# Optimization experiments

Hardware: AMD Instinct MI355X
Metric: run time of the kernel (lower is better)

## Reference

```python
import jax, jax.numpy as jnp
import numpy as np

# SpargeAttn / spas_sage2_attn_meansim block sizes
BLKQ, BLKK = 128, 64
NUM_HEADS = 8
SIMTHRESHD1 = 0.6
CDFTHRESHD = 0.98


def _block_meta(t, blk):
    # t: [B,H,S,D] -> block means [B,H,nb,D] and min-cosine-to-mean per block [B,H,nb]
    B, H, S, D = t.shape
    nb = S // blk
    tb = t.reshape(B, H, nb, blk, D)
    m = tb.mean(axis=3)
    tn = tb / (jnp.linalg.norm(tb, axis=-1, keepdims=True) + 1e-6)
    mn = m / (jnp.linalg.norm(m, axis=-1, keepdims=True) + 1e-6)
    cos = jnp.einsum('bhnkd,bhnd->bhnk', tn, mn)
    return m, cos.min(axis=-1)


def _meansim_sparse_attention(q, k, v, scale):
    # Block-sparse attention with mean-similarity pruning (SpargeAttn meansim).
    qm, qsim = _block_meta(q, BLKQ)          # [B,H,nq,D], [B,H,nq]
    km, ksim = _block_meta(k, BLKK)          # [B,H,nk,D], [B,H,nk]
    q_self = qsim > SIMTHRESHD1              # self-similar Q blocks -> mean is representative
    k_self = ksim > SIMTHRESHD1
    # pooled attention map over block means
    pooled = jax.nn.softmax(jnp.einsum('bhqd,bhkd->bhqk', qm, km) * scale, axis=-1)
    # per Q-block row: keep highest-prob K blocks until cumulative mass >= cdfthreshd
    order = jnp.argsort(-pooled, axis=-1)
    sp = jnp.take_along_axis(pooled, order, axis=-1)
    csum = jnp.cumsum(sp, axis=-1)
    keep_sorted = (csum - sp) < CDFTHRESHD   # always keeps at least the top block
    inv = jnp.argsort(order, axis=-1)
    keep = jnp.take_along_axis(keep_sorted, inv, axis=-1)  # [B,H,nq,nk]
    # conservative fallback: non-self-similar Q/K blocks are never pruned
    block_mask = keep | (~q_self)[..., None] | (~k_self)[:, :, None, :]
    tok_mask = jnp.repeat(jnp.repeat(block_mask, BLKQ, axis=2), BLKK, axis=3)
    s = jnp.einsum('bhqd,bhkd->bhqk', q, k) * scale
    s = jnp.where(tok_mask, s, -jnp.inf)
    p = jax.nn.softmax(s, axis=-1)
    return jnp.einsum('bhqk,bhkd->bhqd', p, v)


def setup_inputs() -> dict:
    key = jax.random.key(0)
    B, L, C = 2, 2048, 512
    ks = jax.random.split(key, 3)
    x = jax.random.normal(ks[0], (B, L, C), jnp.float32)
    Wqkv = jax.random.normal(ks[1], (C, 3 * C), jnp.float32) * (C ** -0.5)
    bqkv = jnp.zeros((3 * C,), jnp.float32)
    Wproj = jax.random.normal(ks[2], (C, C), jnp.float32) * (C ** -0.5)
    bproj = jnp.zeros((C,), jnp.float32)
    return {"x": x, "Wqkv": Wqkv, "bqkv": bqkv, "Wproj": Wproj, "bproj": bproj}


def reference(x, Wqkv, bqkv, Wproj, bproj):
    B, L, C = x.shape
    H = NUM_HEADS
    D = C // H
    scale = D ** -0.5
    qkv = (x @ Wqkv + bqkv).reshape(B, L, 3, H, D)
    qkv = jnp.transpose(qkv, (2, 0, 3, 1, 4))  # [3,B,H,L,D]
    q, k, v = qkv[0], qkv[1], qkv[2]
    o = _meansim_sparse_attention(q, k, v, scale)  # [B,H,L,D]
    o = jnp.transpose(o, (0, 2, 1, 3)).reshape(B, L, C)
    return o @ Wproj + bproj
```

## Files before the change

### kernel.cpp

```cpp
#include <hip/hip_runtime.h>
#include <math.h>

typedef unsigned short ushortT;
typedef unsigned int uintT;
typedef __attribute__((ext_vector_type(8))) short short8;
typedef __attribute__((ext_vector_type(16))) float f32x16;
#define MFMA32(a, b, c) __builtin_amdgcn_mfma_f32_32x32x16_bf16((a), (b), (c), 0, 0, 0)


#define LOG2E 1.4426950408889634f

static __device__ __forceinline__ ushortT f2b(float f) {
    union { float f; uintT u; } v; v.f = f;
    uintT u = v.u;
    u += 0x7fffu + ((u >> 16) & 1u);
    return (ushortT)(u >> 16);
}
static __device__ __forceinline__ uintT pack2(float a, float b) {
    return (uintT)f2b(a) | ((uintT)f2b(b) << 16);
}
static __device__ __forceinline__ uintT pack2t(float a, float b) {
    union { float f; uintT u; } x0, x1; x0.f = a; x1.f = b;
    return __builtin_amdgcn_perm(x1.u, x0.u, 0x07060302u);
}
static __device__ __forceinline__ float blo(uintT u) {
    union { uintT u; float f; } v; v.u = u << 16; return v.f;
}
static __device__ __forceinline__ float bhi(uintT u) {
    union { uintT u; float f; } v; v.u = u & 0xffff0000u; return v.f;
}
static __device__ __forceinline__ f32x16 zero16() {
    f32x16 z;
    #pragma unroll
    for (int i = 0; i < 16; ++i) z[i] = 0.f;
    return z;
}

#define B_N 2
#define H_N 8
#define L_N 2048
#define NQB 16
#define NKB 32

__global__ __launch_bounds__(256) void prep_kernel(
    const float* __restrict__ x, ushortT* __restrict__ xb,
    const float* __restrict__ Wq, ushortT* __restrict__ Wqt,
    const float* __restrict__ Wp, ushortT* __restrict__ Wpt) {
    const int bid = blockIdx.x, t = threadIdx.x;
    __shared__ float tile[32][33];
    if (bid < 2048) {
        int i = (bid * 256 + t) * 4;
        float4 v = *(const float4*)(x + i);
        uint2 o; o.x = pack2(v.x, v.y); o.y = pack2(v.z, v.w);
        *(uint2*)(xb + i) = o;
        return;
    }
    const float* W; ushortT* Wt; int C, c0, r0;
    if (bid < 2816) {
        const int b = bid - 2048;
        W = Wq; Wt = Wqt; C = 1536;
        c0 = (b % 48) * 32; r0 = (b / 48) * 32;
    } else {
        const int b = bid - 2816;
        W = Wp; Wt = Wpt; C = 512;
        c0 = (b & 15) * 32; r0 = (b >> 4) * 32;
    }
    const int tx = t & 31, ty = t >> 5;
    #pragma unroll
    for (int i = 0; i < 4; ++i)
        tile[ty + 8 * i][tx] = W[(size_t)(r0 + ty + 8 * i) * C + c0 + tx];
    __syncthreads();
    #pragma unroll
    for (int i = 0; i < 4; ++i) {
        int rr = ty + 8 * i;
        Wt[(size_t)(c0 + rr) * 512 + r0 + tx] = f2b(tile[tx][rr]);
    }
}

__global__ __launch_bounds__(256) void qkv_gemm_kernel(
    const ushortT* __restrict__ xb, const ushortT* __restrict__ wt,
    const float* __restrict__ bias,
    ushortT* __restrict__ qb, ushortT* __restrict__ kbuf, ushortT* __restrict__ vt,
    float* __restrict__ qm, float* __restrict__ km) {
    __shared__ __align__(16) ushortT As[2][128 * 40];
    __shared__ __align__(16) ushortT Bs[2][128 * 40];
    __shared__ float sumbuf[2][128];
    const int t = threadIdx.x;
    const int l = t & 63, w = t >> 6;
    const int lm = l & 31, lh = l >> 5;
    const int wm = w >> 1, wn = w & 1;
    const int rowbase = blockIdx.y * 128;
    const int colbase = blockIdx.x * 128;

    f32x16 acc[2][2];
    acc[0][0] = zero16(); acc[0][1] = zero16();
    acc[1][0] = zero16(); acc[1][1] = zero16();

    const int r = t >> 1, half = t & 1;
    const ushortT* Ag = xb + (size_t)(rowbase + r) * 512 + half * 16;
    const ushortT* Bg = wt + (size_t)(colbase + r) * 512 + half * 16;
    const int so = r * 40 + half * 16;

    uint4 a0, a1, b0, b1;
    a0 = *(const uint4*)(Ag); a1 = *(const uint4*)(Ag + 8);
    b0 = *(const uint4*)(Bg); b1 = *(const uint4*)(Bg + 8);
    *(uint4*)(&As[0][so]) = a0; *(uint4*)(&As[0][so] + 8) = a1;
    *(uint4*)(&Bs[0][so]) = b0; *(uint4*)(&Bs[0][so] + 8) = b1;

    for (int k0 = 0; k0 < 512; k0 += 32) {
        const int cur = (k0 >> 5) & 1;
        __syncthreads();
        if (k0 < 480) {
            a0 = *(const uint4*)(Ag + k0 + 32); a1 = *(const uint4*)(Ag + k0 + 40);
            b0 = *(const uint4*)(Bg + k0 + 32); b1 = *(const uint4*)(Bg + k0 + 40);
        }
        #pragma unroll
        for (int ks = 0; ks < 2; ++ks) {
            const int ko = 16 * ks + 8 * lh;
            short8 a_0 = *(const short8*)(&As[cur][(64 * wm + lm) * 40 + ko]);
            short8 a_1 = *(const short8*)(&As[cur][(64 * wm + 32 + lm) * 40 + ko]);
            short8 b_0 = *(const short8*)(&Bs[cur][(64 * wn + lm) * 40 + ko]);
            short8 b_1 = *(const short8*)(&Bs[cur][(64 * wn + 32 + lm) * 40 + ko]);
            acc[0][0] = MFMA32(a_0, b_0, acc[0][0]);
            acc[0][1] = MFMA32(a_0, b_1, acc[0][1]);
            acc[1][0] = MFMA32(a_1, b_0, acc[1][0]);
            acc[1][1] = MFMA32(a_1, b_1, acc[1][1]);
        }
        if (k0 < 480) {
            const int nxt = cur ^ 1;
            *(uint4*)(&As[nxt][so]) = a0; *(uint4*)(&As[nxt][so] + 8) = a1;
            *(uint4*)(&Bs[nxt][so]) = b0; *(uint4*)(&Bs[nxt][so] + 8) = b1;
        }
    }

    const int which = blockIdx.x >> 2;
    const int by = blockIdx.y;
    const int b = by >> 4;
    float bias2[2];
    int cc[2], hh[2], dd[2];
    #pragma unroll
    for (int nt = 0; nt < 2; ++nt) {
        cc[nt] = colbase + 64 * wn + 32 * nt + lm;
        bias2[nt] = bias[cc[nt]];
        hh[nt] = (cc[nt] >> 6) & 7;
        dd[nt] = cc[nt] & 63;
    }
    float msum[2] = {0.f, 0.f};
    #pragma unroll
    for (int mt = 0; mt < 2; ++mt) {
        #pragma unroll
        for (int nt = 0; nt < 2; ++nt) {
            const size_t hb = (size_t)(b * 8 + hh[nt]);
            #pragma unroll
            for (int rg = 0; rg < 16; ++rg) {
                const int row_local = 64 * wm + 32 * mt + (rg & 3) + 8 * (rg >> 2) + 4 * lh;
                const int token = rowbase + row_local;
                const int ll = token & 2047;
                float val = acc[mt][nt][rg] + bias2[nt];
                if (which == 0) {
                    val *= 0.125f;
                    msum[nt] += val;
                    qb[(hb * 2048 + ll) * 64 + dd[nt]] = f2b(val * LOG2E);
                } else if (which == 1) {
                    msum[nt] += val;
                    kbuf[(hb * 2048 + ll) * 64 + dd[nt]] = f2b(val);
                } else {
                    vt[hb * 131072 + (size_t)(ll >> 6) * 4096 + dd[nt] * 64 + (ll & 63)] = f2b(val);
                }
            }
        }
    }
    if (which == 0) {
        #pragma unroll
        for (int nt = 0; nt < 2; ++nt) {
            float s = msum[nt] + __shfl_xor(msum[nt], 32);
            if (l < 32) sumbuf[wm][64 * wn + 32 * nt + lm] = s;
        }
        __syncthreads();
        if (t < 128) {
            const int c = colbase + t;
            const int h = (c >> 6) & 7, d = c & 63;
            const int qbi = by & 15;
            qm[((size_t)(b * 8 + h) * 16 + qbi) * 64 + d] =
                (sumbuf[0][t] + sumbuf[1][t]) * (1.0f / 128.0f);
        }
    } else if (which == 1) {
        const int kbi = ((by & 15) << 1) | wm;
        #pragma unroll
        for (int nt = 0; nt < 2; ++nt) {
            float s = msum[nt] + __shfl_xor(msum[nt], 32);
            if (l < 32)
                km[((size_t)(b * 8 + hh[nt]) * 32 + kbi) * 64 + dd[nt]] = s * (1.0f / 64.0f);
        }
    }
}

__global__ __launch_bounds__(256) void cos_kernel(const ushortT* __restrict__ qb,
                                                  const ushortT* __restrict__ kbuf,
                                                  const float* __restrict__ qm,
                                                  const float* __restrict__ km,
                                                  float* __restrict__ qs,
                                                  float* __restrict__ ks) {
    const int bh = blockIdx.y, t = threadIdx.x;
    const int l = t & 63, w = t >> 6;
    __shared__ float mS[64];
    __shared__ float wmin[4];
    if (blockIdx.z == 0) {
        if (blockIdx.x >= 16) return;
        const int qbk = blockIdx.x;
        if (t < 64) mS[t] = qm[((size_t)bh * 16 + qbk) * 64 + t];
        __syncthreads();
        float qn = 0.f;
        #pragma unroll
        for (int d = 0; d < 64; ++d) qn += mS[d] * mS[d];
        qn = sqrtf(qn);
        const int tok = t >> 1, half = t & 1;
        const ushortT* qrow = qb + ((size_t)bh * 2048 + qbk * 128 + tok) * 64 + half * 32;
        float dot = 0.f, nn = 0.f;
        #pragma unroll
        for (int c = 0; c < 4; ++c) {
            uint4 u = *(const uint4*)(qrow + c * 8);
            const int db = half * 32 + c * 8;
            float f0 = blo(u.x), f1 = bhi(u.x), f2 = blo(u.y), f3 = bhi(u.y);
            float f4 = blo(u.z), f5 = bhi(u.z), f6 = blo(u.w), f7 = bhi(u.w);
            dot += f0 * mS[db] + f1 * mS[db + 1] + f2 * mS[db + 2] + f3 * mS[db + 3]
                 + f4 * mS[db + 4] + f5 * mS[db + 5] + f6 * mS[db + 6] + f7 * mS[db + 7];
            nn += f0 * f0 + f1 * f1 + f2 * f2 + f3 * f3 + f4 * f4 + f5 * f5 + f6 * f6 + f7 * f7;
        }
        dot += __shfl_xor(dot, 1);
        nn += __shfl_xor(nn, 1);
        float cosv = dot / ((sqrtf(nn) + 1e-6f) * (qn + 1e-6f));
        #pragma unroll
        for (int off = 1; off < 64; off <<= 1) cosv = fminf(cosv, __shfl_xor(cosv, off));
        if (l == 0) wmin[w] = cosv;
        __syncthreads();
        if (t == 0)
            qs[bh * 16 + qbk] = fminf(fminf(wmin[0], wmin[1]), fminf(wmin[2], wmin[3]));
    } else {
        const int kbk = blockIdx.x;
        if (t < 64) mS[t] = km[((size_t)bh * 32 + kbk) * 64 + t];
        __syncthreads();
        float kn = 0.f;
        #pragma unroll
        for (int d = 0; d < 64; ++d) kn += mS[d] * mS[d];
        kn = sqrtf(kn);
        const int tok = t >> 2, quarter = t & 3;
        const ushortT* krow = kbuf + ((size_t)bh * 2048 + kbk * 64 + tok) * 64 + quarter * 16;
        float dot = 0.f, nn = 0.f;
        #pragma unroll
        for (int c = 0; c < 2; ++c) {
            uint4 u = *(const uint4*)(krow + c * 8);
            const int db = quarter * 16 + c * 8;
            float f0 = blo(u.x), f1 = bhi(u.x), f2 = blo(u.y), f3 = bhi(u.y);
            float f4 = blo(u.z), f5 = bhi(u.z), f6 = blo(u.w), f7 = bhi(u.w);
            dot += f0 * mS[db] + f1 * mS[db + 1] + f2 * mS[db + 2] + f3 * mS[db + 3]
                 + f4 * mS[db + 4] + f5 * mS[db + 5] + f6 * mS[db + 6] + f7 * mS[db + 7];
            nn += f0 * f0 + f1 * f1 + f2 * f2 + f3 * f3 + f4 * f4 + f5 * f5 + f6 * f6 + f7 * f7;
        }
        dot += __shfl_xor(dot, 1); dot += __shfl_xor(dot, 2);
        nn += __shfl_xor(nn, 1); nn += __shfl_xor(nn, 2);
        float cosv = dot / ((sqrtf(nn) + 1e-6f) * (kn + 1e-6f));
        #pragma unroll
        for (int off = 1; off < 64; off <<= 1) cosv = fminf(cosv, __shfl_xor(cosv, off));
        if (l == 0) wmin[w] = cosv;
        __syncthreads();
        if (t == 0)
            ks[bh * 32 + kbk] = fminf(fminf(wmin[0], wmin[1]), fminf(wmin[2], wmin[3]));
    }
}

__global__ __launch_bounds__(512) void mask_kernel(const float* __restrict__ qm,
                                                   const float* __restrict__ km,
                                                   const float* __restrict__ qs,
                                                   const float* __restrict__ ks,
                                                   int* __restrict__ maskp) {
    const int bh = blockIdx.x, t = threadIdx.x;
    __shared__ float qmS[16 * 64];
    __shared__ float kmS[32 * 64];
    __shared__ float pooled[16 * 32];
    __shared__ float pnorm[16 * 32];
    for (int i = t; i < 1024; i += 512) qmS[i] = qm[(size_t)bh * 1024 + i];
    for (int i = t; i < 2048; i += 512) kmS[i] = km[(size_t)bh * 2048 + i];
    __syncthreads();
    {
        const int qbi = t >> 5, kbi = t & 31;
        float dot = 0.f;
        #pragma unroll
        for (int d = 0; d < 64; ++d) dot += qmS[qbi * 64 + d] * kmS[kbi * 64 + d];
        pooled[t] = dot;
    }
    __syncthreads();
    if (t < 16) {
        float mx = -1e30f;
        #pragma unroll
        for (int kb = 0; kb < NKB; ++kb) mx = fmaxf(mx, pooled[t * 32 + kb]);
        float sum = 0.f;
        #pragma unroll
        for (int kb = 0; kb < NKB; ++kb) {
            const float e = expf(pooled[t * 32 + kb] - mx);
            pnorm[t * 32 + kb] = e;
            sum += e;
        }
        const float inv = 1.0f / sum;
        #pragma unroll
        for (int kb = 0; kb < NKB; ++kb) pnorm[t * 32 + kb] *= inv;
    }
    __syncthreads();
    {
        const int row = t >> 5, kb = t & 31;
        const float pk = pnorm[row * 32 + kb];
        float before = 0.f;
        #pragma unroll
        for (int j = 0; j < NKB; ++j) {
            const float pj = pnorm[row * 32 + j];
            if (pj > pk || (pj == pk && j < kb)) before += pj;
        }
        const bool keep = before < 0.98f;
        const bool qfb = !(qs[bh * 16 + row] > 0.6f);
        const bool kfb = !(ks[bh * 32 + kb] > 0.6f);
        maskp[((size_t)bh * 16 + row) * 32 + kb] = (keep || qfb || kfb) ? 1 : 0;
    }
}

__global__ __launch_bounds__(256) void attn_kernel(
    const ushortT* __restrict__ qb, const ushortT* __restrict__ kbuf,
    const ushortT* __restrict__ vt, const int* __restrict__ maskp,
    uintT* __restrict__ pc0, uintT* __restrict__ pc1,
    uintT* __restrict__ pc2, uintT* __restrict__ pc3, float* __restrict__ lp) {
    __shared__ __align__(16) ushortT Ks[2][64 * 72];
    __shared__ __align__(16) ushortT Vs[2][64 * 72];
    __shared__ int klist[33];
    const int t = threadIdx.x;
    const int l = t & 63, w = t >> 6;
    const int lm = l & 31, lh = l >> 5;
    const int qt = blockIdx.x, bh = blockIdx.y, kc = blockIdx.z;
    const int NC = gridDim.z;

    if (w == 0) {
        const int* mrow = maskp + ((size_t)bh * 16 + qt) * 32;
        const int keep = (l < 32) ? mrow[l] : 0;
        unsigned long long bal = __ballot(keep != 0);
        if (keep) {
            const int rank = __popcll(bal & ((1ULL << l) - 1ULL));
            klist[rank] = l;
        }
        if (l == 0) klist[32] = __popcll(bal);
    }
    const ushortT* qg = qb + ((size_t)bh * 2048 + qt * 128) * 64;
    short8 qf[4];
    #pragma unroll
    for (int ksd = 0; ksd < 4; ++ksd)
        qf[ksd] = *(const short8*)(qg + (32 * w + lm) * 64 + 16 * ksd + 8 * lh);
    __syncthreads();

    const int cnt = klist[32];
    const int per = cnt / NC, rem = cnt - per * NC;
    const int n = per + (kc < rem ? 1 : 0);
    const int s = kc * per + (kc < rem ? kc : rem);

    const ushortT* kgb = kbuf + (size_t)bh * 2048 * 64;
    const ushortT* vgb = vt + (size_t)bh * 131072;
    const int cr = t >> 3, cp = (t & 7) * 8;
    const int gK0 = cr * 64 + cp, gK1 = gK0 + 2048;
    const int sK0 = cr * 72 + cp, sK1 = sK0 + 2304;

    f32x16 oacc[2];
    oacc[0] = zero16(); oacc[1] = zero16();
    float l_i = 0.f;

    uint4 ka0, ka1, va0, va1;
    if (n > 0) {
        const int kb0 = klist[s];
        const ushortT* kg = kgb + (size_t)kb0 * 4096;
        const ushortT* vg = vgb + (size_t)kb0 * 4096;
        ka0 = *(const uint4*)(kg + gK0); ka1 = *(const uint4*)(kg + gK1);
        va0 = *(const uint4*)(vg + gK0); va1 = *(const uint4*)(vg + gK1);
        *(uint4*)(&Ks[0][sK0]) = ka0; *(uint4*)(&Ks[0][sK1]) = ka1;
        *(uint4*)(&Vs[0][sK0]) = va0; *(uint4*)(&Vs[0][sK1]) = va1;
    }

    for (int i = 0; i < n; ++i) {
        const int cur = i & 1;
        __syncthreads();
        if (i + 1 < n) {
            const int kbn = klist[s + i + 1];
            const ushortT* kg = kgb + (size_t)kbn * 4096;
            const ushortT* vg = vgb + (size_t)kbn * 4096;
            ka0 = *(const uint4*)(kg + gK0); ka1 = *(const uint4*)(kg + gK1);
            va0 = *(const uint4*)(vg + gK0); va1 = *(const uint4*)(vg + gK1);
        }
        f32x16 sacc[2];
        sacc[0] = zero16(); sacc[1] = zero16();
        #pragma unroll
        for (int ksd = 0; ksd < 4; ++ksd) {
            const int ko = 16 * ksd + 8 * lh;
            short8 kf0 = *(const short8*)(&Ks[cur][lm * 72 + ko]);
            short8 kf1 = *(const short8*)(&Ks[cur][(32 + lm) * 72 + ko]);
            sacc[0] = MFMA32(kf0, qf[ksd], sacc[0]);
            sacc[1] = MFMA32(kf1, qf[ksd], sacc[1]);
        }
        float psum0 = 0.f, psum1 = 0.f;
        uintT uu[2][4][2];
        #pragma unroll
        for (int mt = 0; mt < 2; ++mt) {
            #pragma unroll
            for (int rp = 0; rp < 8; ++rp) {
                const float e0 = exp2f(sacc[mt][2 * rp]);
                const float e1 = exp2f(sacc[mt][2 * rp + 1]);
                psum0 += e0; psum1 += e1;
                uu[mt][rp >> 1][rp & 1] = pack2t(e0, e1);
            }
        }
        float psum = psum0 + psum1;
        psum += __shfl_xor(psum, 32);
        l_i += psum;
        #pragma unroll
        for (int ksk = 0; ksk < 4; ++ksk) {
            const int mt = ksk >> 1, par = ksk & 1;
            const uintT kA = lh ? uu[mt][2 * par + 1][0] : uu[mt][2 * par][0];
            const uintT kB = lh ? uu[mt][2 * par + 1][1] : uu[mt][2 * par][1];
            const uintT sA = lh ? uu[mt][2 * par][0] : uu[mt][2 * par + 1][0];
            const uintT sB = lh ? uu[mt][2 * par][1] : uu[mt][2 * par + 1][1];
            const uintT rA = (uintT)__shfl_xor((int)sA, 32);
            const uintT rB = (uintT)__shfl_xor((int)sB, 32);
            union { uintT u[4]; short8 v; } cv;
            if (lh == 0) { cv.u[0] = kA; cv.u[1] = kB; cv.u[2] = rA; cv.u[3] = rB; }
            else         { cv.u[0] = rA; cv.u[1] = rB; cv.u[2] = kA; cv.u[3] = kB; }
            const int ko = 16 * ksk + 8 * lh;
            short8 vf0 = *(const short8*)(&Vs[cur][lm * 72 + ko]);
            short8 vf1 = *(const short8*)(&Vs[cur][(32 + lm) * 72 + ko]);
            oacc[0] = MFMA32(vf0, cv.v, oacc[0]);
            oacc[1] = MFMA32(vf1, cv.v, oacc[1]);
        }
        if (i + 1 < n) {
            const int nxt = cur ^ 1;
            *(uint4*)(&Ks[nxt][sK0]) = ka0; *(uint4*)(&Ks[nxt][sK1]) = ka1;
            *(uint4*)(&Vs[nxt][sK0]) = va0; *(uint4*)(&Vs[nxt][sK1]) = va1;
        }
    }
    if (lh == 0)
        lp[kc * 32768 + ((size_t)bh * 16 + qt) * 128 + 32 * w + lm] = l_i;
    uintT pu[16];
    #pragma unroll
    for (int mt = 0; mt < 2; ++mt)
        #pragma unroll
        for (int rp = 0; rp < 8; ++rp)
            pu[mt * 8 + rp] = pack2(oacc[mt][2 * rp], oacc[mt][2 * rp + 1]);
    uintT* pcb = (kc == 0) ? pc0 : (kc == 1) ? pc1 : (kc == 2) ? pc2 : pc3;
    uintT* pdst = pcb + (((size_t)bh * 16 + qt) * 4 + w) * 1024 + l * 4;
    #pragma unroll
    for (int i4 = 0; i4 < 4; ++i4)
        *(uint4*)(pdst + i4 * 256) =
            make_uint4(pu[i4 * 4], pu[i4 * 4 + 1], pu[i4 * 4 + 2], pu[i4 * 4 + 3]);
}

__global__ __launch_bounds__(256) void reduce_kernel(
    const uintT* __restrict__ pc0, const uintT* __restrict__ pc1,
    const uintT* __restrict__ pc2, const uintT* __restrict__ pc3,
    const float* __restrict__ lp, ushortT* __restrict__ ob, int NC) {
    const int t = threadIdx.x;
    const int l = t & 63, w = t >> 6;
    const int lm = l & 31, lh = l >> 5;
    const int qt = blockIdx.x, bh = blockIdx.y;
    const size_t base = (((size_t)bh * 16 + qt) * 4 + w) * 1024 + l * 4;
    const int qrow = 32 * w + lm;
    float accL[16], accH[16];
    #pragma unroll
    for (int i = 0; i < 16; ++i) { accL[i] = 0.f; accH[i] = 0.f; }
    float lsum = 0.f;
    #pragma unroll
    for (int c = 0; c < 4; ++c) {
        if (c >= NC) break;
        const uintT* p = (c == 0) ? pc0 : (c == 1) ? pc1 : (c == 2) ? pc2 : pc3;
        #pragma unroll
        for (int i4 = 0; i4 < 4; ++i4) {
            uint4 v = *(const uint4*)(p + base + i4 * 256);
            accL[i4 * 4 + 0] += blo(v.x); accH[i4 * 4 + 0] += bhi(v.x);
            accL[i4 * 4 + 1] += blo(v.y); accH[i4 * 4 + 1] += bhi(v.y);
            accL[i4 * 4 + 2] += blo(v.z); accH[i4 * 4 + 2] += bhi(v.z);
            accL[i4 * 4 + 3] += blo(v.w); accH[i4 * 4 + 3] += bhi(v.w);
        }
        lsum += lp[c * 32768 + ((size_t)bh * 16 + qt) * 128 + qrow];
    }
    const float invl = 1.0f / lsum;
    __syncthreads();
    ushortT* orow = ob + ((size_t)bh * 2048 + qt * 128 + qrow) * 64;
    #pragma unroll
    for (int idx = 0; idx < 16; ++idx) {
        const int mt = idx >> 3, rp = idx & 7;
        const int d0 = 32 * mt + 8 * (rp >> 1) + 4 * lh + 2 * (rp & 1);
        *(uintT*)(orow + d0) = pack2(accL[idx] * invl, accH[idx] * invl);
    }
}

__global__ __launch_bounds__(256) void proj_gemm_kernel(
    const ushortT* __restrict__ ob, const ushortT* __restrict__ wpt,
    const float* __restrict__ bias, float* __restrict__ out) {
    __shared__ __align__(16) ushortT As[2][128 * 40];
    __shared__ __align__(16) ushortT Bs[2][64 * 40];
    const int t = threadIdx.x;
    const int l = t & 63, w = t >> 6;
    const int lm = l & 31, lh = l >> 5;
    const int rowbase = blockIdx.y * 128;
    const int colbase = blockIdx.x * 64;

    f32x16 acc[2];
    acc[0] = zero16(); acc[1] = zero16();

    const int r = t >> 1, half = t & 1;
    const int token = rowbase + r;
    const int b2 = token >> 11, lt = token & 2047;
    const int soA = r * 40 + half * 16;
    const ushortT* obbase = ob + ((size_t)(b2 * 8) * 2048 + lt) * 64 + half * 16;
    const int rb = t >> 2, q4 = t & 3;
    const int soB = rb * 40 + q4 * 8;
    const ushortT* Bg = wpt + (size_t)(colbase + rb) * 512 + q4 * 8;

    uint4 a0, a1, b0;
    a0 = *(const uint4*)(obbase); a1 = *(const uint4*)(obbase + 8);
    b0 = *(const uint4*)(Bg);
    *(uint4*)(&As[0][soA]) = a0; *(uint4*)(&As[0][soA] + 8) = a1;
    *(uint4*)(&Bs[0][soB]) = b0;

    for (int k0 = 0; k0 < 512; k0 += 32) {
        const int cur = (k0 >> 5) & 1;
        __syncthreads();
        if (k0 < 480) {
            const int kn = k0 + 32;
            const ushortT* Ag = obbase + (size_t)(kn >> 6) * 131072 + (kn & 63);
            a0 = *(const uint4*)(Ag); a1 = *(const uint4*)(Ag + 8);
            b0 = *(const uint4*)(Bg + kn);
        }
        #pragma unroll
        for (int ks = 0; ks < 2; ++ks) {
            const int ko = 16 * ks + 8 * lh;
            short8 af = *(const short8*)(&As[cur][(32 * w + lm) * 40 + ko]);
            short8 b_0 = *(const short8*)(&Bs[cur][lm * 40 + ko]);
            short8 b_1 = *(const short8*)(&Bs[cur][(32 + lm) * 40 + ko]);
            acc[0] = MFMA32(af, b_0, acc[0]);
            acc[1] = MFMA32(af, b_1, acc[1]);
        }
        if (k0 < 480) {
            const int nxt = cur ^ 1;
            *(uint4*)(&As[nxt][soA]) = a0; *(uint4*)(&As[nxt][soA] + 8) = a1;
            *(uint4*)(&Bs[nxt][soB]) = b0;
        }
    }
    float bias2[2];
    #pragma unroll
    for (int nt = 0; nt < 2; ++nt) bias2[nt] = bias[colbase + 32 * nt + lm];
    #pragma unroll
    for (int nt = 0; nt < 2; ++nt) {
        const int c = colbase + 32 * nt + lm;
        #pragma unroll
        for (int rg = 0; rg < 16; ++rg) {
            const int row_local = 32 * w + (rg & 3) + 8 * (rg >> 2) + 4 * lh;
            out[(size_t)(rowbase + row_local) * 512 + c] = acc[nt][rg] + bias2[nt];
        }
    }
}

extern "C" void kernel_launch(void* const* d_in, const int* in_sizes, int n_in,
                              void* d_out, int out_size, void* d_ws, size_t ws_size,
                              hipStream_t stream) {
    const float* x     = (const float*)d_in[0];
    const float* Wqkv  = (const float*)d_in[1];
    const float* bqkv  = (const float*)d_in[2];
    const float* Wproj = (const float*)d_in[3];
    const float* bproj = (const float*)d_in[4];
    float* out = (float*)d_out;

    char* w = (char*)d_ws;
    ushortT* xb     = (ushortT*)(w);
    ushortT* wqkvt  = (ushortT*)(w + 4194304);
    ushortT* wprojt = (ushortT*)(w + 5767168);
    ushortT* qb     = (ushortT*)(w + 6291456);
    ushortT* kbuf   = (ushortT*)(w + 10485760);
    ushortT* vt     = (ushortT*)(w + 14680064);
    ushortT* ob     = (ushortT*)(w + 18874368);
    float*   qm     = (float*)(w + 23068672);
    float*   km     = (float*)(w + 23134208);
    float*   qs     = (float*)(w + 23265280);
    float*   ks     = (float*)(w + 23266304);
    int*     maskp  = (int*)(w + 23268352);
    float*   lp2    = (float*)(w + 23301120);
    uintT*   pc2    = (uintT*)(w + 23563264);
    uintT*   pc3    = (uintT*)(w + 27757568);
    float*   lp4    = (float*)(w + 31951872);
    const int NC = (ws_size >= 32476160) ? 4 : 2;
    float* lpA = (NC == 4) ? lp4 : lp2;

    uintT* pc0 = (uintT*)xb;
    uintT* pc1 = (uintT*)ob;
    if (NC == 2) { pc2 = pc0; pc3 = pc0; }

    prep_kernel<<<3072, 256, 0, stream>>>(x, xb, Wqkv, wqkvt, Wproj, wprojt);
    qkv_gemm_kernel<<<dim3(12, 32), 256, 0, stream>>>(xb, wqkvt, bqkv, qb, kbuf, vt, qm, km);
    cos_kernel<<<dim3(32, 16, 2), 256, 0, stream>>>(qb, kbuf, qm, km, qs, ks);
    mask_kernel<<<16, 512, 0, stream>>>(qm, km, qs, ks, maskp);
    attn_kernel<<<dim3(16, 16, NC), 256, 0, stream>>>(qb, kbuf, vt, maskp, pc0, pc1, pc2, pc3, lpA);
    reduce_kernel<<<dim3(16, 16), 256, 0, stream>>>(pc0, pc1, pc2, pc3, lpA, ob, NC);
    proj_gemm_kernel<<<dim3(8, 32), 256, 0, stream>>>(ob, wprojt, bproj, out);
}
```

Before: 158.2 us.

## Shrink GEMM tiles, drop LDS staging in attention, swap attention grid order

The QKV GEMM moves from 128x128 to 128x64 tiles, so the grid doubles and each block covers exactly one head, which simplifies the mean-reduction epilogue. The projection GEMM moves to 64x64 tiles with one MFMA accumulator per wave, doubling its grid. The attention kernel drops the double-buffered shared-memory K/V staging and reads K/V fragments directly from global memory, and swaps grid x/y so consecutive blocks share a query tile across heads. The aim is more parallelism and less LDS and sync overhead, at the cost of less data reuse and uncoalesced, unpipelined global loads in attention.

```diff
diff --git a/kernel.cpp b/kernel.cpp
--- a/kernel.cpp
+++ b/kernel.cpp
@@ -83,114 +83,101 @@
     ushortT* __restrict__ qb, ushortT* __restrict__ kbuf, ushortT* __restrict__ vt,
     float* __restrict__ qm, float* __restrict__ km) {
     __shared__ __align__(16) ushortT As[2][128 * 40];
-    __shared__ __align__(16) ushortT Bs[2][128 * 40];
-    __shared__ float sumbuf[2][128];
+    __shared__ __align__(16) ushortT Bs[2][64 * 40];
+    __shared__ float sumbuf[4][64];
     const int t = threadIdx.x;
     const int l = t & 63, w = t >> 6;
     const int lm = l & 31, lh = l >> 5;
-    const int wm = w >> 1, wn = w & 1;
     const int rowbase = blockIdx.y * 128;
-    const int colbase = blockIdx.x * 128;
-
-    f32x16 acc[2][2];
-    acc[0][0] = zero16(); acc[0][1] = zero16();
-    acc[1][0] = zero16(); acc[1][1] = zero16();
+    const int colbase = blockIdx.x * 64;
+
+    f32x16 acc[2];
+    acc[0] = zero16(); acc[1] = zero16();
 
     const int r = t >> 1, half = t & 1;
     const ushortT* Ag = xb + (size_t)(rowbase + r) * 512 + half * 16;
-    const ushortT* Bg = wt + (size_t)(colbase + r) * 512 + half * 16;
-    const int so = r * 40 + half * 16;
-
-    uint4 a0, a1, b0, b1;
+    const int soA = r * 40 + half * 16;
+    const int rb = t >> 2, q4 = t & 3;
+    const ushortT* Bg = wt + (size_t)(colbase + rb) * 512 + q4 * 8;
+    const int soB = rb * 40 + q4 * 8;
+
+    uint4 a0, a1, b0;
     a0 = *(const uint4*)(Ag); a1 = *(const uint4*)(Ag + 8);
-    b0 = *(const uint4*)(Bg); b1 = *(const uint4*)(Bg + 8);
-    *(uint4*)(&As[0][so]) = a0; *(uint4*)(&As[0][so] + 8) = a1;
-    *(uint4*)(&Bs[0][so]) = b0; *(uint4*)(&Bs[0][so] + 8) = b1;
+    b0 = *(const uint4*)(Bg);
+    *(uint4*)(&As[0][soA]) = a0; *(uint4*)(&As[0][soA] + 8) = a1;
+    *(uint4*)(&Bs[0][soB]) = b0;
 
     for (int k0 = 0; k0 < 512; k0 += 32) {
         const int cur = (k0 >> 5) & 1;
         __syncthreads();
         if (k0 < 480) {
             a0 = *(const uint4*)(Ag + k0 + 32); a1 = *(const uint4*)(Ag + k0 + 40);
-            b0 = *(const uint4*)(Bg + k0 + 32); b1 = *(const uint4*)(Bg + k0 + 40);
+            b0 = *(const uint4*)(Bg + k0 + 32);
         }
         #pragma unroll
         for (int ks = 0; ks < 2; ++ks) {
             const int ko = 16 * ks + 8 * lh;
-            short8 a_0 = *(const short8*)(&As[cur][(64 * wm + lm) * 40 + ko]);
-            short8 a_1 = *(const short8*)(&As[cur][(64 * wm + 32 + lm) * 40 + ko]);
-            short8 b_0 = *(const short8*)(&Bs[cur][(64 * wn + lm) * 40 + ko]);
-            short8 b_1 = *(const short8*)(&Bs[cur][(64 * wn + 32 + lm) * 40 + ko]);
-            acc[0][0] = MFMA32(a_0, b_0, acc[0][0]);
-            acc[0][1] = MFMA32(a_0, b_1, acc[0][1]);
-            acc[1][0] = MFMA32(a_1, b_0, acc[1][0]);
-            acc[1][1] = MFMA32(a_1, b_1, acc[1][1]);
+            short8 af  = *(const short8*)(&As[cur][(32 * w + lm) * 40 + ko]);
+            short8 b_0 = *(const short8*)(&Bs[cur][lm * 40 + ko]);
+            short8 b_1 = *(const short8*)(&Bs[cur][(32 + lm) * 40 + ko]);
+            acc[0] = MFMA32(af, b_0, acc[0]);
+            acc[1] = MFMA32(af, b_1, acc[1]);
         }
         if (k0 < 480) {
             const int nxt = cur ^ 1;
-            *(uint4*)(&As[nxt][so]) = a0; *(uint4*)(&As[nxt][so] + 8) = a1;
-            *(uint4*)(&Bs[nxt][so]) = b0; *(uint4*)(&Bs[nxt][so] + 8) = b1;
-        }
-    }
-
-    const int which = blockIdx.x >> 2;
+            *(uint4*)(&As[nxt][soA]) = a0; *(uint4*)(&As[nxt][soA] + 8) = a1;
+            *(uint4*)(&Bs[nxt][soB]) = b0;
+        }
+    }
+
+    const int which = blockIdx.x >> 3;
+    const int h = blockIdx.x & 7;
     const int by = blockIdx.y;
     const int b = by >> 4;
+    const size_t hb = (size_t)(b * 8 + h);
     float bias2[2];
-    int cc[2], hh[2], dd[2];
+    #pragma unroll
+    for (int nt = 0; nt < 2; ++nt) bias2[nt] = bias[colbase + 32 * nt + lm];
+    float msum[2] = {0.f, 0.f};
     #pragma unroll
     for (int nt = 0; nt < 2; ++nt) {
-        cc[nt] = colbase + 64 * wn + 32 * nt + lm;
-        bias2[nt] = bias[cc[nt]];
-        hh[nt] = (cc[nt] >> 6) & 7;
-        dd[nt] = cc[nt] & 63;
-    }
-    float msum[2] = {0.f, 0.f};
-    #pragma unroll
-    for (int mt = 0; mt < 2; ++mt) {
-        #pragma unroll
-        for (int nt = 0; nt < 2; ++nt) {
-            const size_t hb = (size_t)(b * 8 + hh[nt]);
-            #pragma unroll
-            for (int rg = 0; rg < 16; ++rg) {
-                const int row_local = 64 * wm + 32 * mt + (rg & 3) + 8 * (rg >> 2) + 4 * lh;
-                const int token = rowbase + row_local;
-                const int ll = token & 2047;
-                float val = acc[mt][nt][rg] + bias2[nt];
-                if (which == 0) {
-                    val *= 0.125f;
-                    msum[nt] += val;
-                    qb[(hb * 2048 + ll) * 64 + dd[nt]] = f2b(val * LOG2E);
-                } else if (which == 1) {
-                    msum[nt] += val;
-                    kbuf[(hb * 2048 + ll) * 64 + dd[nt]] = f2b(val);
-                } else {
-                    vt[hb * 131072 + (size_t)(ll >> 6) * 4096 + dd[nt] * 64 + (ll & 63)] = f2b(val);
-                }
+        const int dd = 32 * nt + lm;
+        #pragma unroll
+        for (int rg = 0; rg < 16; ++rg) {
+            const int row_local = 32 * w + (rg & 3) + 8 * (rg >> 2) + 4 * lh;
+            const int ll = (rowbase + row_local) & 2047;
+            float val = acc[nt][rg] + bias2[nt];
+            if (which == 0) {
+                val *= 0.125f;
+                msum[nt] += val;
+                qb[(hb * 2048 + ll) * 64 + dd] = f2b(val * LOG2E);
+            } else if (which == 1) {
+                msum[nt] += val;
+                kbuf[(hb * 2048 + ll) * 64 + dd] = f2b(val);
+            } else {
+                vt[hb * 131072 + (size_t)(ll >> 6) * 4096 + dd * 64 + (ll & 63)] = f2b(val);
             }
         }
     }
+    if (which == 2) return;
+    #pragma unroll
+    for (int nt = 0; nt < 2; ++nt) {
+        float s = msum[nt] + __shfl_xor(msum[nt], 32);
+        if (l < 32) sumbuf[w][32 * nt + lm] = s;
+    }
+    __syncthreads();
     if (which == 0) {
-        #pragma unroll
-        for (int nt = 0; nt < 2; ++nt) {
-            float s = msum[nt] + __shfl_xor(msum[nt], 32);
-            if (l < 32) sumbuf[wm][64 * wn + 32 * nt + lm] = s;
-        }
-        __syncthreads();
+        if (t < 64) {
+            const int qbi = by & 15;
+            qm[(hb * 16 + qbi) * 64 + t] =
+                (sumbuf[0][t] + sumbuf[1][t] + sumbuf[2][t] + sumbuf[3][t]) * (1.0f / 128.0f);
+        }
+    } else {
         if (t < 128) {
-            const int c = colbase + t;
-            const int h = (c >> 6) & 7, d = c & 63;
-            const int qbi = by & 15;
-            qm[((size_t)(b * 8 + h) * 16 + qbi) * 64 + d] =
-                (sumbuf[0][t] + sumbuf[1][t]) * (1.0f / 128.0f);
-        }
-    } else if (which == 1) {
-        const int kbi = ((by & 15) << 1) | wm;
-        #pragma unroll
-        for (int nt = 0; nt < 2; ++nt) {
-            float s = msum[nt] + __shfl_xor(msum[nt], 32);
-            if (l < 32)
-                km[((size_t)(b * 8 + hh[nt]) * 32 + kbi) * 64 + dd[nt]] = s * (1.0f / 64.0f);
+            const int d = t & 63, pair = t >> 6;
+            const int kbi = 2 * (by & 15) + pair;
+            km[(hb * 32 + kbi) * 64 + d] =
+                (sumbuf[2 * pair][d] + sumbuf[2 * pair + 1][d]) * (1.0f / 64.0f);
         }
     }
 }
@@ -327,13 +314,11 @@
     const ushortT* __restrict__ vt, const int* __restrict__ maskp,
     uintT* __restrict__ pc0, uintT* __restrict__ pc1,
     uintT* __restrict__ pc2, uintT* __restrict__ pc3, float* __restrict__ lp) {
-    __shared__ __align__(16) ushortT Ks[2][64 * 72];
-    __shared__ __align__(16) ushortT Vs[2][64 * 72];
     __shared__ int klist[33];
     const int t = threadIdx.x;
     const int l = t & 63, w = t >> 6;
     const int lm = l & 31, lh = l >> 5;
-    const int qt = blockIdx.x, bh = blockIdx.y, kc = blockIdx.z;
+    const int bh = blockIdx.x, qt = blockIdx.y, kc = blockIdx.z;
     const int NC = gridDim.z;
 
     if (w == 0) {
@@ -358,46 +343,29 @@
     const int n = per + (kc < rem ? 1 : 0);
     const int s = kc * per + (kc < rem ? kc : rem);
 
-    const ushortT* kgb = kbuf + (size_t)bh * 2048 * 64;
+    const ushortT* kgb = kbuf + (size_t)bh * 131072;
     const ushortT* vgb = vt + (size_t)bh * 131072;
-    const int cr = t >> 3, cp = (t & 7) * 8;
-    const int gK0 = cr * 64 + cp, gK1 = gK0 + 2048;
-    const int sK0 = cr * 72 + cp, sK1 = sK0 + 2304;
 
     f32x16 oacc[2];
     oacc[0] = zero16(); oacc[1] = zero16();
     float l_i = 0.f;
 
-    uint4 ka0, ka1, va0, va1;
-    if (n > 0) {
-        const int kb0 = klist[s];
-        const ushortT* kg = kgb + (size_t)kb0 * 4096;
-        const ushortT* vg = vgb + (size_t)kb0 * 4096;
-        ka0 = *(const uint4*)(kg + gK0); ka1 = *(const uint4*)(kg + gK1);
-        va0 = *(const uint4*)(vg + gK0); va1 = *(const uint4*)(vg + gK1);
-        *(uint4*)(&Ks[0][sK0]) = ka0; *(uint4*)(&Ks[0][sK1]) = ka1;
-        *(uint4*)(&Vs[0][sK0]) = va0; *(uint4*)(&Vs[0][sK1]) = va1;
-    }
-
     for (int i = 0; i < n; ++i) {
-        const int cur = i & 1;
-        __syncthreads();
-        if (i + 1 < n) {
-            const int kbn = klist[s + i + 1];
-            const ushortT* kg = kgb + (size_t)kbn * 4096;
-            const ushortT* vg = vgb + (size_t)kbn * 4096;
-            ka0 = *(const uint4*)(kg + gK0); ka1 = *(const uint4*)(kg + gK1);
-            va0 = *(const uint4*)(vg + gK0); va1 = *(const uint4*)(vg + gK1);
+        const int kb = klist[s + i];
+        const ushortT* kg = kgb + (size_t)kb * 4096;
+        const ushortT* vg = vgb + (size_t)kb * 4096;
+        short8 kf0[4], kf1[4];
+        #pragma unroll
+        for (int ksd = 0; ksd < 4; ++ksd) {
+            kf0[ksd] = *(const short8*)(kg + lm * 64 + 16 * ksd + 8 * lh);
+            kf1[ksd] = *(const short8*)(kg + (32 + lm) * 64 + 16 * ksd + 8 * lh);
         }
         f32x16 sacc[2];
         sacc[0] = zero16(); sacc[1] = zero16();
         #pragma unroll
         for (int ksd = 0; ksd < 4; ++ksd) {
-            const int ko = 16 * ksd + 8 * lh;
-            short8 kf0 = *(const short8*)(&Ks[cur][lm * 72 + ko]);
-            short8 kf1 = *(const short8*)(&Ks[cur][(32 + lm) * 72 + ko]);
-            sacc[0] = MFMA32(kf0, qf[ksd], sacc[0]);
-            sacc[1] = MFMA32(kf1, qf[ksd], sacc[1]);
+            sacc[0] = MFMA32(kf0[ksd], qf[ksd], sacc[0]);
+            sacc[1] = MFMA32(kf1[ksd], qf[ksd], sacc[1]);
         }
         float psum0 = 0.f, psum1 = 0.f;
         uintT uu[2][4][2];
@@ -427,15 +395,10 @@
             if (lh == 0) { cv.u[0] = kA; cv.u[1] = kB; cv.u[2] = rA; cv.u[3] = rB; }
             else         { cv.u[0] = rA; cv.u[1] = rB; cv.u[2] = kA; cv.u[3] = kB; }
             const int ko = 16 * ksk + 8 * lh;
-            short8 vf0 = *(const short8*)(&Vs[cur][lm * 72 + ko]);
-            short8 vf1 = *(const short8*)(&Vs[cur][(32 + lm) * 72 + ko]);
+            short8 vf0 = *(const short8*)(vg + lm * 64 + ko);
+            short8 vf1 = *(const short8*)(vg + (32 + lm) * 64 + ko);
             oacc[0] = MFMA32(vf0, cv.v, oacc[0]);
             oacc[1] = MFMA32(vf1, cv.v, oacc[1]);
-        }
-        if (i + 1 < n) {
-            const int nxt = cur ^ 1;
-            *(uint4*)(&Ks[nxt][sK0]) = ka0; *(uint4*)(&Ks[nxt][sK1]) = ka1;
-            *(uint4*)(&Vs[nxt][sK0]) = va0; *(uint4*)(&Vs[nxt][sK1]) = va1;
         }
     }
     if (lh == 0)
@@ -496,31 +459,29 @@
 __global__ __launch_bounds__(256) void proj_gemm_kernel(
     const ushortT* __restrict__ ob, const ushortT* __restrict__ wpt,
     const float* __restrict__ bias, float* __restrict__ out) {
-    __shared__ __align__(16) ushortT As[2][128 * 40];
+    __shared__ __align__(16) ushortT As[2][64 * 40];
     __shared__ __align__(16) ushortT Bs[2][64 * 40];
     const int t = threadIdx.x;
     const int l = t & 63, w = t >> 6;
     const int lm = l & 31, lh = l >> 5;
-    const int rowbase = blockIdx.y * 128;
+    const int rh = w & 1, ch = w >> 1;
+    const int rowbase = blockIdx.y * 64;
     const int colbase = blockIdx.x * 64;
 
-    f32x16 acc[2];
-    acc[0] = zero16(); acc[1] = zero16();
-
-    const int r = t >> 1, half = t & 1;
+    f32x16 acc = zero16();
+
+    const int r = t >> 2, q4 = t & 3;
     const int token = rowbase + r;
     const int b2 = token >> 11, lt = token & 2047;
-    const int soA = r * 40 + half * 16;
-    const ushortT* obbase = ob + ((size_t)(b2 * 8) * 2048 + lt) * 64 + half * 16;
-    const int rb = t >> 2, q4 = t & 3;
-    const int soB = rb * 40 + q4 * 8;
-    const ushortT* Bg = wpt + (size_t)(colbase + rb) * 512 + q4 * 8;
-
-    uint4 a0, a1, b0;
-    a0 = *(const uint4*)(obbase); a1 = *(const uint4*)(obbase + 8);
+    const int so = r * 40 + q4 * 8;
+    const ushortT* obbase = ob + ((size_t)(b2 * 8) * 2048 + lt) * 64 + q4 * 8;
+    const ushortT* Bg = wpt + (size_t)(colbase + r) * 512 + q4 * 8;
+
+    uint4 a0, b0;
+    a0 = *(const uint4*)(obbase);
     b0 = *(const uint4*)(Bg);
-    *(uint4*)(&As[0][soA]) = a0; *(uint4*)(&As[0][soA] + 8) = a1;
-    *(uint4*)(&Bs[0][soB]) = b0;
+    *(uint4*)(&As[0][so]) = a0;
+    *(uint4*)(&Bs[0][so]) = b0;
 
     for (int k0 = 0; k0 < 512; k0 += 32) {
         const int cur = (k0 >> 5) & 1;
@@ -528,35 +489,28 @@
         if (k0 < 480) {
             const int kn = k0 + 32;
             const ushortT* Ag = obbase + (size_t)(kn >> 6) * 131072 + (kn & 63);
-            a0 = *(const uint4*)(Ag); a1 = *(const uint4*)(Ag + 8);
+            a0 = *(const uint4*)(Ag);
             b0 = *(const uint4*)(Bg + kn);
         }
         #pragma unroll
         for (int ks = 0; ks < 2; ++ks) {
             const int ko = 16 * ks + 8 * lh;
-            short8 af = *(const short8*)(&As[cur][(32 * w + lm) * 40 + ko]);
-            short8 b_0 = *(const short8*)(&Bs[cur][lm * 40 + ko]);
-            short8 b_1 = *(const short8*)(&Bs[cur][(32 + lm) * 40 + ko]);
-            acc[0] = MFMA32(af, b_0, acc[0]);
-            acc[1] = MFMA32(af, b_1, acc[1]);
+            short8 af = *(const short8*)(&As[cur][(32 * rh + lm) * 40 + ko]);
+            short8 bf = *(const short8*)(&Bs[cur][(32 * ch + lm) * 40 + ko]);
+            acc = MFMA32(af, bf, acc);
         }
         if (k0 < 480) {
             const int nxt = cur ^ 1;
-            *(uint4*)(&As[nxt][soA]) = a0; *(uint4*)(&As[nxt][soA] + 8) = a1;
-            *(uint4*)(&Bs[nxt][soB]) = b0;
-        }
-    }
-    float bias2[2];
-    #pragma unroll
-    for (int nt = 0; nt < 2; ++nt) bias2[nt] = bias[colbase + 32 * nt + lm];
-    #pragma unroll
-    for (int nt = 0; nt < 2; ++nt) {
-        const int c = colbase + 32 * nt + lm;
-        #pragma unroll
-        for (int rg = 0; rg < 16; ++rg) {
-            const int row_local = 32 * w + (rg & 3) + 8 * (rg >> 2) + 4 * lh;
-            out[(size_t)(rowbase + row_local) * 512 + c] = acc[nt][rg] + bias2[nt];
-        }
+            *(uint4*)(&As[nxt][so]) = a0;
+            *(uint4*)(&Bs[nxt][so]) = b0;
+        }
+    }
+    const int c = colbase + 32 * ch + lm;
+    const float bb = bias[c];
+    #pragma unroll
+    for (int rg = 0; rg < 16; ++rg) {
+        const int row_local = 32 * rh + (rg & 3) + 8 * (rg >> 2) + 4 * lh;
+        out[(size_t)(rowbase + row_local) * 512 + c] = acc[rg] + bb;
     }
 }
 
@@ -595,10 +549,10 @@
     if (NC == 2) { pc2 = pc0; pc3 = pc0; }
 
     prep_kernel<<<3072, 256, 0, stream>>>(x, xb, Wqkv, wqkvt, Wproj, wprojt);
-    qkv_gemm_kernel<<<dim3(12, 32), 256, 0, stream>>>(xb, wqkvt, bqkv, qb, kbuf, vt, qm, km);
+    qkv_gemm_kernel<<<dim3(24, 32), 256, 0, stream>>>(xb, wqkvt, bqkv, qb, kbuf, vt, qm, km);
     cos_kernel<<<dim3(32, 16, 2), 256, 0, stream>>>(qb, kbuf, qm, km, qs, ks);
     mask_kernel<<<16, 512, 0, stream>>>(qm, km, qs, ks, maskp);
     attn_kernel<<<dim3(16, 16, NC), 256, 0, stream>>>(qb, kbuf, vt, maskp, pc0, pc1, pc2, pc3, lpA);
     reduce_kernel<<<dim3(16, 16), 256, 0, stream>>>(pc0, pc1, pc2, pc3, lpA, ob, NC);
-    proj_gemm_kernel<<<dim3(8, 32), 256, 0, stream>>>(ob, wprojt, bproj, out);
-}
+    proj_gemm_kernel<<<dim3(8, 64), 256, 0, stream>>>(ob, wprojt, bproj, out);
+}
```

After: 185.1 us. +17.0%, slower.
